# Kernel optimization log

Measured on AMD Instinct MI355X. Metric: run time of the kernel, lower is better.

Reference implementation:

```python
import jax, jax.numpy as jnp
import numpy as np
import math

B, T, D, H = 4, 2048, 1024, 16
DH = D // H


def setup_inputs() -> dict:
    key = jax.random.key(0)
    k1, k2, k3 = jax.random.split(key, 3)
    x = jax.random.normal(k1, (B, T, D), dtype=jnp.float32)
    # causal mask: True = masked (positions j > i)
    attn_mask = jnp.triu(jnp.ones((T, T), dtype=bool), k=1)
    key_padding_mask = jnp.zeros((B, T), dtype=bool)  # no padding
    W_qkv = jax.random.normal(k2, (D, 3 * D), dtype=jnp.float32) / math.sqrt(D)
    W_out = jax.random.normal(k3, (D, D), dtype=jnp.float32) / math.sqrt(D)
    return {"x": x, "W_qkv": W_qkv, "W_out": W_out,
            "attn_mask": attn_mask, "key_padding_mask": key_padding_mask}


def reference(x, W_qkv, W_out, attn_mask, key_padding_mask):
    # qkv projection (bias=False)
    qkv = x @ W_qkv                                   # [B,T,3D]
    q, k, v = jnp.split(qkv, 3, axis=-1)              # each [B,T,D]
    # reshape to heads: [B,H,T,DH]
    q = q.reshape(B, T, H, DH).transpose(0, 2, 1, 3)
    k = k.reshape(B, T, H, DH).transpose(0, 2, 1, 3)
    v = v.reshape(B, T, H, DH).transpose(0, 2, 1, 3)
    scale = 1.0 / math.sqrt(DH)
    scores = jnp.einsum('bhqd,bhkd->bhqk', q, k) * scale   # [B,H,T,T]
    neg_inf = jnp.float32(-jnp.inf)
    scores = jnp.where(attn_mask[None, None, :, :], neg_inf, scores)
    scores = jnp.where(key_padding_mask[:, None, None, :], neg_inf, scores)
    attn = jax.nn.softmax(scores, axis=-1)            # dropout p=0.0 -> identity
    out = jnp.einsum('bhqk,bhkd->bhqd', attn, v)      # [B,H,T,DH]
    out = out.transpose(0, 2, 1, 3).reshape(B, T, D)
    return out @ W_out
```

## Files before the change

kernel.cpp:

```cpp
#include <hip/hip_runtime.h>
#include <hip/hip_bf16.h>

#define Bsz 4
#define T 2048
#define D 1024
#define H 16
#define DH 64

typedef unsigned short u16;
typedef __attribute__((ext_vector_type(8))) __bf16 bf16x8;
typedef __attribute__((ext_vector_type(4))) float f32x4;

__device__ inline u16 f2bf(float f) {
  union { float f; unsigned u; } v; v.f = f;
  unsigned r = (v.u + 0x7FFFu + ((v.u >> 16) & 1u)) >> 16;
  return (u16)r;
}
__device__ inline unsigned pack_bf16(float a, float b) {
  union { float f; unsigned u; } A, B; A.f = a; B.f = b;
  unsigned au = A.u + 0x8000u, bu = B.u + 0x8000u;
  return __builtin_amdgcn_perm(bu, au, 0x07060302);
}

__device__ inline void gll16(const u16* g, u16* l) {
  __builtin_amdgcn_global_load_lds((const __attribute__((address_space(1))) void*)g,
                                   (__attribute__((address_space(3))) void*)l, 16, 0, 0);
}

__global__ __launch_bounds__(256) void convert_f32_bf16(const float* __restrict__ in,
                                                        u16* __restrict__ out, int n4) {
  int i = blockIdx.x * 256 + threadIdx.x;
  if (i < n4) {
    float4 v = reinterpret_cast<const float4*>(in)[i];
    ushort4 o;
    o.x = f2bf(v.x); o.y = f2bf(v.y); o.z = f2bf(v.z); o.w = f2bf(v.w);
    reinterpret_cast<ushort4*>(out)[i] = o;
  }
}

__global__ __launch_bounds__(256) void transpose_f32_bf16(const float* __restrict__ in,
                                                          u16* __restrict__ out, int K, int N) {
  __shared__ float tile[32][33];
  int tx = threadIdx.x & 31, ty = threadIdx.x >> 5;
  int n0 = blockIdx.x * 32, k0 = blockIdx.y * 32;
  #pragma unroll
  for (int i = 0; i < 4; ++i)
    tile[ty + i * 8][tx] = in[(size_t)(k0 + ty + i * 8) * N + n0 + tx];
  __syncthreads();
  #pragma unroll
  for (int i = 0; i < 4; ++i)
    out[(size_t)(n0 + ty + i * 8) * K + k0 + tx] = f2bf(tile[tx][ty + i * 8]);
}

template <int MODE>
__global__ __launch_bounds__(512, 2) void gemm256(const u16* __restrict__ A, const u16* __restrict__ BT,
                                                  float* __restrict__ C,
                                                  u16* __restrict__ Qh, u16* __restrict__ Kh,
                                                  u16* __restrict__ VTh, int M, int N, int K) {
  __shared__ alignas(16) u16 SA[2][256][64];
  __shared__ alignas(16) u16 SB[2][192][64];
  int tid = threadIdx.x;

  int flat = blockIdx.y * gridDim.x + blockIdx.x;
  int cpx = (int)(gridDim.x * gridDim.y) >> 3;
  int nf = (flat & 7) * cpx + (flat >> 3);
  int bx = nf % (int)gridDim.x, by = nf / (int)gridDim.x;
  int m0 = by * 256, n0 = bx * 192;

  int w = tid >> 6, lane = tid & 63;
  int llo = lane & 15, lhi = lane >> 4;
  int wr = w >> 2, wc = w & 3;

  int cs0 = ((lhi ^ (llo & 7)) << 3);
  int cs1 = (((4 + lhi) ^ (llo & 7)) << 3);

  int srcCol = (((lane & 7) ^ ((lane >> 3) & 7)) << 3);
  const u16* gAl = A + (size_t)(m0 + w * 8 + (lane >> 3)) * K + srcCol;
  const u16* gBl = BT + (size_t)(n0 + w * 8 + (lane >> 3)) * K + srcCol;

  f32x4 acc[8][3];
  #pragma unroll
  for (int i = 0; i < 8; ++i)
    #pragma unroll
    for (int j = 0; j < 3; ++j) acc[i][j] = (f32x4){0.f, 0.f, 0.f, 0.f};

  int nt = K >> 6;

  auto stA = [&](int buf, int c, int kt) {
    gll16(gAl + (size_t)(c * 64) * K + kt * 64, &SA[buf][c * 64 + w * 8][0]);
  };
  auto stB = [&](int buf, int c, int kt) {
    gll16(gBl + (size_t)(c * 64) * K + kt * 64, &SB[buf][c * 64 + w * 8][0]);
  };

  stA(0, 0, 0); stA(0, 1, 0); stA(0, 2, 0); stA(0, 3, 0);
  stB(0, 0, 0); stB(0, 1, 0); stB(0, 2, 0);
  asm volatile("s_waitcnt vmcnt(0)" ::: "memory");
  __builtin_amdgcn_s_barrier();
  __builtin_amdgcn_sched_barrier(0);

  bf16x8 aA[4][2], bB[3][2];

  #pragma unroll 2
  for (int t = 0; t < nt; ++t) {
    int p = t & 1;

    #pragma unroll
    for (int i = 0; i < 4; ++i) {
      aA[i][0] = *reinterpret_cast<const bf16x8*>(&SA[p][wr * 128 + i * 16 + llo][cs0]);
      aA[i][1] = *reinterpret_cast<const bf16x8*>(&SA[p][wr * 128 + i * 16 + llo][cs1]);
    }
    #pragma unroll
    for (int j = 0; j < 2; ++j) {
      bB[j][0] = *reinterpret_cast<const bf16x8*>(&SB[p][wc * 48 + j * 16 + llo][cs0]);
      bB[j][1] = *reinterpret_cast<const bf16x8*>(&SB[p][wc * 48 + j * 16 + llo][cs1]);
    }
    if (t + 1 < nt) { stA(1 - p, 0, t + 1); stA(1 - p, 2, t + 1); }
    __builtin_amdgcn_s_barrier();
    asm volatile("s_waitcnt lgkmcnt(0)" ::: "memory");
    __builtin_amdgcn_sched_barrier(0);
    __builtin_amdgcn_s_setprio(1);
    #pragma unroll
    for (int i = 0; i < 4; ++i)
      #pragma unroll
      for (int j = 0; j < 2; ++j) {
        acc[i][j] = __builtin_amdgcn_mfma_f32_16x16x32_bf16(aA[i][0], bB[j][0], acc[i][j], 0, 0, 0);
        acc[i][j] = __builtin_amdgcn_mfma_f32_16x16x32_bf16(aA[i][1], bB[j][1], acc[i][j], 0, 0, 0);
      }
    __builtin_amdgcn_s_setprio(0);
    __builtin_amdgcn_s_barrier();
    __builtin_amdgcn_sched_barrier(0);

    bB[2][0] = *reinterpret_cast<const bf16x8*>(&SB[p][wc * 48 + 32 + llo][cs0]);
    bB[2][1] = *reinterpret_cast<const bf16x8*>(&SB[p][wc * 48 + 32 + llo][cs1]);
    if (t + 1 < nt) { stB(1 - p, 0, t + 1); stB(1 - p, 1, t + 1); }
    __builtin_amdgcn_s_barrier();
    asm volatile("s_waitcnt lgkmcnt(0)" ::: "memory");
    __builtin_amdgcn_sched_barrier(0);
    __builtin_amdgcn_s_setprio(1);
    #pragma unroll
    for (int i = 0; i < 4; ++i) {
      acc[i][2] = __builtin_amdgcn_mfma_f32_16x16x32_bf16(aA[i][0], bB[2][0], acc[i][2], 0, 0, 0);
      acc[i][2] = __builtin_amdgcn_mfma_f32_16x16x32_bf16(aA[i][1], bB[2][1], acc[i][2], 0, 0, 0);
    }
    __builtin_amdgcn_s_setprio(0);
    if (t + 1 < nt) asm volatile("s_waitcnt vmcnt(4)" ::: "memory");
    else            asm volatile("s_waitcnt vmcnt(0)" ::: "memory");
    __builtin_amdgcn_s_barrier();
    __builtin_amdgcn_sched_barrier(0);

    #pragma unroll
    for (int i = 0; i < 4; ++i) {
      aA[i][0] = *reinterpret_cast<const bf16x8*>(&SA[p][wr * 128 + 64 + i * 16 + llo][cs0]);
      aA[i][1] = *reinterpret_cast<const bf16x8*>(&SA[p][wr * 128 + 64 + i * 16 + llo][cs1]);
    }
    if (t + 1 < nt) { stB(1 - p, 2, t + 1); stA(1 - p, 1, t + 1); }
    __builtin_amdgcn_s_barrier();
    asm volatile("s_waitcnt lgkmcnt(0)" ::: "memory");
    __builtin_amdgcn_sched_barrier(0);
    __builtin_amdgcn_s_setprio(1);
    #pragma unroll
    for (int i = 0; i < 4; ++i)
      #pragma unroll
      for (int j = 0; j < 2; ++j) {
        acc[4 + i][j] = __builtin_amdgcn_mfma_f32_16x16x32_bf16(aA[i][0], bB[j][0], acc[4 + i][j], 0, 0, 0);
        acc[4 + i][j] = __builtin_amdgcn_mfma_f32_16x16x32_bf16(aA[i][1], bB[j][1], acc[4 + i][j], 0, 0, 0);
      }
    __builtin_amdgcn_s_setprio(0);
    __builtin_amdgcn_s_barrier();
    __builtin_amdgcn_sched_barrier(0);

    if (t + 1 < nt) stA(1 - p, 3, t + 1);
    __builtin_amdgcn_s_setprio(1);
    #pragma unroll
    for (int i = 0; i < 4; ++i) {
      acc[4 + i][2] = __builtin_amdgcn_mfma_f32_16x16x32_bf16(aA[i][0], bB[2][0], acc[4 + i][2], 0, 0, 0);
      acc[4 + i][2] = __builtin_amdgcn_mfma_f32_16x16x32_bf16(aA[i][1], bB[2][1], acc[4 + i][2], 0, 0, 0);
    }
    __builtin_amdgcn_s_setprio(0);
    if (t + 1 < nt) asm volatile("s_waitcnt vmcnt(2)" ::: "memory");
    __builtin_amdgcn_s_barrier();
    __builtin_amdgcn_sched_barrier(0);
  }

  if (MODE == 0) {
    #pragma unroll
    for (int i = 0; i < 8; ++i) {
      int ml = m0 + wr * 128 + i * 16 + lhi * 4;
      #pragma unroll
      for (int j = 0; j < 3; ++j) {
        int nl = n0 + wc * 48 + j * 16 + llo;
        #pragma unroll
        for (int r = 0; r < 4; ++r)
          C[(size_t)(ml + r) * N + nl] = acc[i][j][r];
      }
    }
  } else {
    #pragma unroll
    for (int i = 0; i < 8; ++i) {
      int mbase = m0 + wr * 128 + i * 16 + lhi * 4;
      int t0 = mbase & (T - 1);
      int b_ = mbase >> 11;
      #pragma unroll
      for (int j = 0; j < 3; ++j) {
        int nl = n0 + wc * 48 + j * 16 + llo;
        int seg = (n0 + wc * 48 + j * 16) >> 10;
        int h = (nl >> 6) & 15, d = nl & 63;
        int bh = b_ * H + h;
        if (seg == 0) {
          #pragma unroll
          for (int r = 0; r < 4; ++r)
            Qh[((size_t)bh * T + t0 + r) * DH + d] = f2bf(acc[i][j][r] * 0.125f);
        } else if (seg == 1) {
          #pragma unroll
          for (int r = 0; r < 4; ++r)
            Kh[((size_t)bh * T + t0 + r) * DH + d] = f2bf(acc[i][j][r]);
        } else {
          uint2 p;
          p.x = pack_bf16(acc[i][j][0], acc[i][j][1]);
          p.y = pack_bf16(acc[i][j][2], acc[i][j][3]);
          *reinterpret_cast<uint2*>(&VTh[((size_t)bh * DH + d) * T + t0]) = p;
        }
      }
    }
  }
}

template <int MODE>
__global__ __launch_bounds__(256) void gemm128(const u16* __restrict__ A, const u16* __restrict__ BT,
                                               float* __restrict__ C,
                                               u16* __restrict__ Qh, u16* __restrict__ Kh,
                                               u16* __restrict__ VTh, int M, int N, int K) {
  __shared__ u16 As[128][32];
  __shared__ u16 Bs[128][32];
  int tid = threadIdx.x;
  int m0 = blockIdx.y * 128, n0 = blockIdx.x * 128;
  int w = tid >> 6, lane = tid & 63;
  int llo = lane & 15, lhi = lane >> 4;
  int wm = (w >> 1) * 64, wn = (w & 1) * 64;

  f32x4 acc[4][4];
  #pragma unroll
  for (int i = 0; i < 4; ++i)
    #pragma unroll
    for (int j = 0; j < 4; ++j) acc[i][j] = (f32x4){0.f, 0.f, 0.f, 0.f};

  const u16* gA = A + (size_t)(m0 + w * 32 + (lane >> 2)) * K + (lane & 3) * 8;
  const u16* gB = BT + (size_t)(n0 + w * 32 + (lane >> 2)) * K + (lane & 3) * 8;

  for (int k0 = 0; k0 < K; k0 += 32) {
    gll16(gA + k0, &As[w * 32][0]);
    gll16(gA + (size_t)16 * K + k0, &As[w * 32 + 16][0]);
    gll16(gB + k0, &Bs[w * 32][0]);
    gll16(gB + (size_t)16 * K + k0, &Bs[w * 32 + 16][0]);
    __syncthreads();
    bf16x8 af[4], bfr[4];
    #pragma unroll
    for (int i = 0; i < 4; ++i)
      af[i] = *reinterpret_cast<const bf16x8*>(&As[wm + i * 16 + llo][lhi * 8]);
    #pragma unroll
    for (int j = 0; j < 4; ++j)
      bfr[j] = *reinterpret_cast<const bf16x8*>(&Bs[wn + j * 16 + llo][lhi * 8]);
    #pragma unroll
    for (int i = 0; i < 4; ++i)
      #pragma unroll
      for (int j = 0; j < 4; ++j)
        acc[i][j] = __builtin_amdgcn_mfma_f32_16x16x32_bf16(af[i], bfr[j], acc[i][j], 0, 0, 0);
    __syncthreads();
  }

  if (MODE == 0) {
    #pragma unroll
    for (int i = 0; i < 4; ++i)
      #pragma unroll
      for (int j = 0; j < 4; ++j) {
        int nl = n0 + wn + j * 16 + llo;
        #pragma unroll
        for (int r = 0; r < 4; ++r) {
          int ml = m0 + wm + i * 16 + lhi * 4 + r;
          C[(size_t)ml * N + nl] = acc[i][j][r];
        }
      }
  }
}

__global__ __launch_bounds__(1024, 4) void attn_fwd(const u16* __restrict__ Qh, const u16* __restrict__ Kh,
                                                    const u16* __restrict__ VTh, u16* __restrict__ AO) {
  __shared__ u16 QP[16][16][72];
  __shared__ u16 Ks[64][72];
  __shared__ u16 Vs[64][72];
  int tid = threadIdx.x;
  int qp = blockIdx.x, bh = blockIdx.y;
  int w = tid >> 6, lane = tid & 63;
  int llo = lane & 15, lhi = lane >> 4;

  int qrow_s = tid >> 2, qc = tid & 3;
  int krow_s = tid >> 4, kc = tid & 15;
  const u16* kbase = Kh + ((size_t)bh * T + krow_s) * DH + kc * 4;
  const u16* vbase = VTh + ((size_t)bh * DH + krow_s) * T + kc * 4;
  int b = bh >> 4, h = bh & 15;

  #pragma unroll 1
  for (int half = 0; half < 2; ++half) {
    int qt = half ? (7 - qp) : qp;
    int q0 = qt * 256;

    bf16x8 aq[2];
    {
      const uint4* g = reinterpret_cast<const uint4*>(
          Qh + ((size_t)bh * T + q0 + qrow_s) * DH + qc * 16);
      uint4 a = g[0], bb = g[1];
      uint4* dst = reinterpret_cast<uint4*>(&QP[w][qrow_s & 15][qc * 16]);
      dst[0] = a; dst[1] = bb;
      #pragma unroll
      for (int ks = 0; ks < 2; ++ks)
        aq[ks] = *reinterpret_cast<const bf16x8*>(&QP[w][llo][ks * 32 + lhi * 8]);
    }

    f32x4 o[4];
    #pragma unroll
    for (int i = 0; i < 4; ++i) o[i] = (f32x4){0.f, 0.f, 0.f, 0.f};
    float l_run = 0.f;

    int nj = 4 * qt + 4;
    uint2 ka = *reinterpret_cast<const uint2*>(kbase);
    uint2 va = *reinterpret_cast<const uint2*>(vbase);

    #pragma unroll 1
    for (int j = 0; j < nj; ++j) {
      __syncthreads();
      *reinterpret_cast<uint2*>(&Ks[krow_s][kc * 4]) = ka;
      *reinterpret_cast<uint2*>(&Vs[krow_s][kc * 4]) = va;
      if (j + 1 < nj) {
        ka = *reinterpret_cast<const uint2*>(kbase + (size_t)(j + 1) * 64 * DH);
        va = *reinterpret_cast<const uint2*>(vbase + (j + 1) * 64);
      } else if (half == 0) {
        ka = *reinterpret_cast<const uint2*>(kbase);
        va = *reinterpret_cast<const uint2*>(vbase);
      }
      __syncthreads();

      if (q0 + w * 16 + 15 >= j * 64) {
        f32x4 sc[4];
        #pragma unroll
        for (int kt = 0; kt < 4; ++kt) {
          bf16x8 bk0 = *reinterpret_cast<const bf16x8*>(&Ks[kt * 16 + llo][lhi * 8]);
          bf16x8 bk1 = *reinterpret_cast<const bf16x8*>(&Ks[kt * 16 + llo][32 + lhi * 8]);
          f32x4 z = (f32x4){0.f, 0.f, 0.f, 0.f};
          f32x4 t0 = __builtin_amdgcn_mfma_f32_16x16x32_bf16(bk0, aq[0], z, 0, 0, 0);
          sc[kt] = __builtin_amdgcn_mfma_f32_16x16x32_bf16(bk1, aq[1], t0, 0, 0, 0);
        }

        if (j >= 4 * qt) {
          int qrow_g = q0 + w * 16 + llo;
          #pragma unroll
          for (int kt = 0; kt < 4; ++kt)
            #pragma unroll
            for (int r = 0; r < 4; ++r) {
              int key_g = j * 64 + kt * 16 + lhi * 4 + r;
              if (key_g > qrow_g) sc[kt][r] = -__builtin_inff();
            }
        }

        float s_sum = 0.f;
        #pragma unroll
        for (int kt = 0; kt < 4; ++kt)
          #pragma unroll
          for (int r = 0; r < 4; ++r) {
            float p = __expf(sc[kt][r]);
            sc[kt][r] = p;
            s_sum += p;
          }
        s_sum += __shfl_xor(s_sum, 16);
        s_sum += __shfl_xor(s_sum, 32);
        l_run += s_sum;

        #pragma unroll
        for (int kt = 0; kt < 4; ++kt) {
          uint2 p;
          p.x = pack_bf16(sc[kt][0], sc[kt][1]);
          p.y = pack_bf16(sc[kt][2], sc[kt][3]);
          *reinterpret_cast<uint2*>(&QP[w][llo][kt * 16 + lhi * 4]) = p;
        }

        #pragma unroll
        for (int kk2 = 0; kk2 < 2; ++kk2) {
          bf16x8 pa = *reinterpret_cast<const bf16x8*>(&QP[w][llo][kk2 * 32 + lhi * 8]);
          #pragma unroll
          for (int nt = 0; nt < 4; ++nt) {
            bf16x8 bv = *reinterpret_cast<const bf16x8*>(&Vs[nt * 16 + llo][kk2 * 32 + lhi * 8]);
            o[nt] = __builtin_amdgcn_mfma_f32_16x16x32_bf16(pa, bv, o[nt], 0, 0, 0);
          }
        }
      }
    }

    #pragma unroll
    for (int r = 0; r < 4; ++r) {
      float inv = 1.f / __shfl(l_run, lhi * 4 + r);
      int t = q0 + w * 16 + lhi * 4 + r;
      #pragma unroll
      for (int nt = 0; nt < 4; ++nt)
        AO[((size_t)(b * T + t)) * D + h * 64 + nt * 16 + llo] = f2bf(o[nt][r] * inv);
    }
  }
}

extern "C" void kernel_launch(void* const* d_in, const int* in_sizes, int n_in,
                              void* d_out, int out_size, void* d_ws, size_t ws_size,
                              hipStream_t stream) {
  (void)in_sizes; (void)n_in; (void)out_size;
  const float* x = (const float*)d_in[0];
  const float* Wqkv = (const float*)d_in[1];
  const float* Wout = (const float*)d_in[2];
  float* out = (float*)d_out;

  char* ws = (char*)d_ws;
  size_t off = 0;
  u16* xb = (u16*)(ws + off);    off += (size_t)Bsz * T * D * 2;
  u16* WqkvT = (u16*)(ws + off); off += (size_t)3 * D * D * 2;
  u16* WoutT = (u16*)(ws + off); off += (size_t)D * D * 2;
  u16* Qh = (u16*)(ws + off);    off += (size_t)Bsz * H * T * DH * 2;
  u16* Kh = (u16*)(ws + off);    off += (size_t)Bsz * H * T * DH * 2;
  u16* VTh = (u16*)(ws + off);   off += (size_t)Bsz * H * DH * T * 2;
  u16* AO = xb;
  if (ws_size < off) return;

  int n4 = Bsz * T * D / 4;
  convert_f32_bf16<<<(n4 + 255) / 256, 256, 0, stream>>>(x, xb, n4);
  transpose_f32_bf16<<<dim3(3 * D / 32, D / 32), 256, 0, stream>>>(Wqkv, WqkvT, D, 3 * D);
  transpose_f32_bf16<<<dim3(D / 32, D / 32), 256, 0, stream>>>(Wout, WoutT, D, D);
  gemm256<1><<<dim3(3 * D / 192, Bsz * T / 256), 512, 0, stream>>>(xb, WqkvT, nullptr, Qh, Kh, VTh,
                                                                   Bsz * T, 3 * D, D);
  attn_fwd<<<dim3(4, Bsz * H), 1024, 0, stream>>>(Qh, Kh, VTh, AO);
  gemm128<0><<<dim3(D / 128, Bsz * T / 128), 256, 0, stream>>>(AO, WoutT, out, nullptr, nullptr, nullptr,
                                                               Bsz * T, D, D);
}
```

Baseline: 271.9 us.

## Halve attention query tile, double grid, and XOR-swizzle LDS instead of padding

```diff
diff --git a/kernel.cpp b/kernel.cpp
--- a/kernel.cpp
+++ b/kernel.cpp
@@ -284,37 +284,40 @@
   }
 }
 
-__global__ __launch_bounds__(1024, 4) void attn_fwd(const u16* __restrict__ Qh, const u16* __restrict__ Kh,
-                                                    const u16* __restrict__ VTh, u16* __restrict__ AO) {
-  __shared__ u16 QP[16][16][72];
-  __shared__ u16 Ks[64][72];
-  __shared__ u16 Vs[64][72];
+__global__ __launch_bounds__(512, 4) void attn_fwd(const u16* __restrict__ Qh, const u16* __restrict__ Kh,
+                                                   const u16* __restrict__ VTh, u16* __restrict__ AO) {
+  __shared__ u16 QP[8][16][64];
+  __shared__ u16 Ks[64][64];
+  __shared__ u16 Vs[64][64];
   int tid = threadIdx.x;
   int qp = blockIdx.x, bh = blockIdx.y;
   int w = tid >> 6, lane = tid & 63;
   int llo = lane & 15, lhi = lane >> 4;
+  int swz = llo & 7;
 
   int qrow_s = tid >> 2, qc = tid & 3;
-  int krow_s = tid >> 4, kc = tid & 15;
-  const u16* kbase = Kh + ((size_t)bh * T + krow_s) * DH + kc * 4;
-  const u16* vbase = VTh + ((size_t)bh * DH + krow_s) * T + kc * 4;
+  int krow_s = tid >> 3, kc = tid & 7;
+  int kvcol = ((kc ^ (krow_s & 7)) << 3);
+  const u16* kbase = Kh + ((size_t)bh * T + krow_s) * DH + kc * 8;
+  const u16* vbase = VTh + ((size_t)bh * DH + krow_s) * T + kc * 8;
   int b = bh >> 4, h = bh & 15;
 
   #pragma unroll 1
   for (int half = 0; half < 2; ++half) {
-    int qt = half ? (7 - qp) : qp;
-    int q0 = qt * 256;
+    int qt = half ? (15 - qp) : qp;
+    int q0 = qt * 128;
 
     bf16x8 aq[2];
     {
       const uint4* g = reinterpret_cast<const uint4*>(
           Qh + ((size_t)bh * T + q0 + qrow_s) * DH + qc * 16);
       uint4 a = g[0], bb = g[1];
-      uint4* dst = reinterpret_cast<uint4*>(&QP[w][qrow_s & 15][qc * 16]);
-      dst[0] = a; dst[1] = bb;
+      int r7 = qrow_s & 7;
+      *reinterpret_cast<uint4*>(&QP[w][qrow_s & 15][((2 * qc) ^ r7) << 3]) = a;
+      *reinterpret_cast<uint4*>(&QP[w][qrow_s & 15][((2 * qc + 1) ^ r7) << 3]) = bb;
       #pragma unroll
       for (int ks = 0; ks < 2; ++ks)
-        aq[ks] = *reinterpret_cast<const bf16x8*>(&QP[w][llo][ks * 32 + lhi * 8]);
+        aq[ks] = *reinterpret_cast<const bf16x8*>(&QP[w][llo][((ks * 4 + lhi) ^ swz) << 3]);
     }
 
     f32x4 o[4];
@@ -322,21 +325,21 @@
     for (int i = 0; i < 4; ++i) o[i] = (f32x4){0.f, 0.f, 0.f, 0.f};
     float l_run = 0.f;
 
-    int nj = 4 * qt + 4;
-    uint2 ka = *reinterpret_cast<const uint2*>(kbase);
-    uint2 va = *reinterpret_cast<const uint2*>(vbase);
+    int nj = 2 * qt + 2;
+    uint4 ka = *reinterpret_cast<const uint4*>(kbase);
+    uint4 va = *reinterpret_cast<const uint4*>(vbase);
 
     #pragma unroll 1
     for (int j = 0; j < nj; ++j) {
       __syncthreads();
-      *reinterpret_cast<uint2*>(&Ks[krow_s][kc * 4]) = ka;
-      *reinterpret_cast<uint2*>(&Vs[krow_s][kc * 4]) = va;
+      *reinterpret_cast<uint4*>(&Ks[krow_s][kvcol]) = ka;
+      *reinterpret_cast<uint4*>(&Vs[krow_s][kvcol]) = va;
       if (j + 1 < nj) {
-        ka = *reinterpret_cast<const uint2*>(kbase + (size_t)(j + 1) * 64 * DH);
-        va = *reinterpret_cast<const uint2*>(vbase + (j + 1) * 64);
+        ka = *reinterpret_cast<const uint4*>(kbase + (size_t)(j + 1) * 64 * DH);
+        va = *reinterpret_cast<const uint4*>(vbase + (j + 1) * 64);
       } else if (half == 0) {
-        ka = *reinterpret_cast<const uint2*>(kbase);
-        va = *reinterpret_cast<const uint2*>(vbase);
+        ka = *reinterpret_cast<const uint4*>(kbase);
+        va = *reinterpret_cast<const uint4*>(vbase);
       }
       __syncthreads();
 
@@ -344,14 +347,14 @@
         f32x4 sc[4];
         #pragma unroll
         for (int kt = 0; kt < 4; ++kt) {
-          bf16x8 bk0 = *reinterpret_cast<const bf16x8*>(&Ks[kt * 16 + llo][lhi * 8]);
-          bf16x8 bk1 = *reinterpret_cast<const bf16x8*>(&Ks[kt * 16 + llo][32 + lhi * 8]);
+          bf16x8 bk0 = *reinterpret_cast<const bf16x8*>(&Ks[kt * 16 + llo][(lhi ^ swz) << 3]);
+          bf16x8 bk1 = *reinterpret_cast<const bf16x8*>(&Ks[kt * 16 + llo][((4 + lhi) ^ swz) << 3]);
           f32x4 z = (f32x4){0.f, 0.f, 0.f, 0.f};
           f32x4 t0 = __builtin_amdgcn_mfma_f32_16x16x32_bf16(bk0, aq[0], z, 0, 0, 0);
           sc[kt] = __builtin_amdgcn_mfma_f32_16x16x32_bf16(bk1, aq[1], t0, 0, 0, 0);
         }
 
-        if (j >= 4 * qt) {
+        if (j >= 2 * qt) {
           int qrow_g = q0 + w * 16 + llo;
           #pragma unroll
           for (int kt = 0; kt < 4; ++kt)
@@ -380,15 +383,16 @@
           uint2 p;
           p.x = pack_bf16(sc[kt][0], sc[kt][1]);
           p.y = pack_bf16(sc[kt][2], sc[kt][3]);
-          *reinterpret_cast<uint2*>(&QP[w][llo][kt * 16 + lhi * 4]) = p;
+          *reinterpret_cast<uint2*>(
+              &QP[w][llo][(((2 * kt + (lhi >> 1)) ^ swz) << 3) + (lhi & 1) * 4]) = p;
         }
 
         #pragma unroll
         for (int kk2 = 0; kk2 < 2; ++kk2) {
-          bf16x8 pa = *reinterpret_cast<const bf16x8*>(&QP[w][llo][kk2 * 32 + lhi * 8]);
+          bf16x8 pa = *reinterpret_cast<const bf16x8*>(&QP[w][llo][((kk2 * 4 + lhi) ^ swz) << 3]);
           #pragma unroll
           for (int nt = 0; nt < 4; ++nt) {
-            bf16x8 bv = *reinterpret_cast<const bf16x8*>(&Vs[nt * 16 + llo][kk2 * 32 + lhi * 8]);
+            bf16x8 bv = *reinterpret_cast<const bf16x8*>(&Vs[nt * 16 + llo][((kk2 * 4 + lhi) ^ swz) << 3]);
             o[nt] = __builtin_amdgcn_mfma_f32_16x16x32_bf16(pa, bv, o[nt], 0, 0, 0);
           }
         }
@@ -432,7 +436,7 @@
   transpose_f32_bf16<<<dim3(D / 32, D / 32), 256, 0, stream>>>(Wout, WoutT, D, D);
   gemm256<1><<<dim3(3 * D / 192, Bsz * T / 256), 512, 0, stream>>>(xb, WqkvT, nullptr, Qh, Kh, VTh,
                                                                    Bsz * T, 3 * D, D);
-  attn_fwd<<<dim3(4, Bsz * H), 1024, 0, stream>>>(Qh, Kh, VTh, AO);
+  attn_fwd<<<dim3(8, Bsz * H), 512, 0, stream>>>(Qh, Kh, VTh, AO);
   gemm128<0><<<dim3(D / 128, Bsz * T / 128), 256, 0, stream>>>(AO, WoutT, out, nullptr, nullptr, nullptr,
                                                                Bsz * T, D, D);
 }
```

Result: faster. 263.7 us (-3.0%).
